# Kernel optimization log

Measured on AMD Instinct MI355X. Metric: run time of the kernel, lower is better.

Reference implementation:

```python
import jax, jax.numpy as jnp
import numpy as np

N, E, F_IN, EDIM, HEADS, DIM = 100000, 1600000, 128, 16, 4, 16
HC = HEADS * DIM


def add_self_loops_mean(src, dst, ea, n):
    # PyG add_self_loops with fill_value='mean': self-loop edge_attr is the mean
    # of incoming-edge attrs per target node (0 for isolated nodes).
    cnt = jax.ops.segment_sum(jnp.ones((dst.shape[0],), ea.dtype), dst, num_segments=n)
    sm = jax.ops.segment_sum(ea, dst, num_segments=n)
    loop = jnp.where(cnt[:, None] > 0, sm / jnp.maximum(cnt, 1.0)[:, None], 0.0)
    idx = jnp.arange(n, dtype=src.dtype)
    return (jnp.concatenate([src, idx]), jnp.concatenate([dst, idx]),
            jnp.concatenate([ea, loop], axis=0))


def gatv2(x, src, dst, ea, Wl, bl, Wr, br, We, att, bias):
    n = x.shape[0]
    h, c = att.shape
    xl = (x @ Wl + bl).reshape(n, h, c)   # source transform (lin_l)
    xr = (x @ Wr + br).reshape(n, h, c)   # target transform (lin_r)
    ee = (ea @ We).reshape(-1, h, c)      # edge transform (lin_edge, no bias)
    s = jax.nn.leaky_relu(xl[src] + xr[dst] + ee, negative_slope=0.2)  # [E,h,c]
    alpha = jnp.einsum('ehc,hc->eh', s, att)                           # [E,h]
    amax = jax.ops.segment_max(alpha, dst, num_segments=n)
    amax = jnp.where(jnp.isfinite(amax), amax, 0.0)
    ex = jnp.exp(alpha - amax[dst])
    denom = jax.ops.segment_sum(ex, dst, num_segments=n)
    a = ex / (denom[dst] + 1e-16)                                      # segment softmax
    out = jax.ops.segment_sum(xl[src] * a[:, :, None], dst, num_segments=n)
    return out.reshape(n, h * c) + bias


def setup_inputs() -> dict:
    key = jax.random.key(0)
    ks = jax.random.split(key, 24)
    s = 0.1
    d = {
        'x': jax.random.normal(ks[0], (N, F_IN), jnp.float32),
        'edge_index': jax.random.randint(ks[1], (2, E), 0, N, jnp.int32),
        'edge_attr': jax.random.normal(ks[2], (E, EDIM), jnp.float32),
        'Wl1': jax.random.normal(ks[3], (F_IN, HC)) * s, 'bl1': jnp.zeros((HC,)),
        'Wr1': jax.random.normal(ks[4], (F_IN, HC)) * s, 'br1': jnp.zeros((HC,)),
        'We1': jax.random.normal(ks[5], (EDIM, HC)) * s,
        'att1': jax.random.normal(ks[6], (HEADS, DIM)) * s,
        'bias1': jnp.zeros((HC,)),
        'Wl2': jax.random.normal(ks[7], (HC, HC)) * s, 'bl2': jnp.zeros((HC,)),
        'Wr2': jax.random.normal(ks[8], (HC, HC)) * s, 'br2': jnp.zeros((HC,)),
        'We2': jax.random.normal(ks[9], (EDIM, HC)) * s,
        'att2': jax.random.normal(ks[10], (HEADS, DIM)) * s,
        'bias2': jnp.zeros((HC,)),
        'W_lin1': jax.random.normal(ks[11], (HC, DIM)) * s, 'b_lin1': jnp.zeros((DIM,)),
        'W_lin2': jax.random.normal(ks[12], (DIM, 1)) * s, 'b_lin2': jnp.zeros((1,)),
    }
    return d


def reference(x, edge_index, edge_attr, Wl1, bl1, Wr1, br1, We1, att1, bias1,
              Wl2, bl2, Wr2, br2, We2, att2, bias2,
              W_lin1, b_lin1, W_lin2, b_lin2):
    src, dst, ea = add_self_loops_mean(edge_index[0], edge_index[1], edge_attr, x.shape[0])
    h = jax.nn.relu(gatv2(x, src, dst, ea, Wl1, bl1, Wr1, br1, We1, att1, bias1))
    h = jax.nn.relu(gatv2(h, src, dst, ea, Wl2, bl2, Wr2, br2, We2, att2, bias2))
    h = jax.nn.relu(h @ W_lin1 + b_lin1)
    # dropout p=0.1 is identity in eval mode
    out = jax.nn.sigmoid((h @ W_lin2 + b_lin2)[:, 0])
    return out
```

## Files before the change

### kernel.cpp

```cpp
#include <hip/hip_runtime.h>
#include <stdint.h>

typedef unsigned short u16;
typedef unsigned int u32;
typedef unsigned long long u64;

typedef __attribute__((ext_vector_type(8))) short bfrag;
typedef __attribute__((ext_vector_type(4))) float f32x4;
typedef __attribute__((ext_vector_type(2))) float f32x2;

__device__ __forceinline__ float bf2f(u16 u) { return __uint_as_float(((u32)u) << 16); }
__device__ __forceinline__ u16 f2bf(float f) {
    u32 i = __float_as_uint(f);
    u32 r = i + 0x7fffu + ((i >> 16) & 1u);
    return (u16)(r >> 16);
}
__device__ __forceinline__ float lo16(u32 u) { return __uint_as_float(u << 16); }
__device__ __forceinline__ float hi16(u32 u) { return __uint_as_float(u & 0xffff0000u); }
__device__ __forceinline__ u32 pack2(float a, float b) {
    return (u32)f2bf(a) | ((u32)f2bf(b) << 16);
}
#define RFL(x) __builtin_amdgcn_readfirstlane(x)

#define DPP_ROR_ADD(p, ctrl) \
    p += __int_as_float(__builtin_amdgcn_update_dpp(0, __float_as_int(p), ctrl, 0xF, 0xF, false))
__device__ __forceinline__ float red16(float p) {
    DPP_ROR_ADD(p, 0x128);
    DPP_ROR_ADD(p, 0x124);
    DPP_ROR_ADD(p, 0x122);
    DPP_ROR_ADD(p, 0x121);
    return p;
}

__global__ void deg_hist(const int* __restrict__ dst, int E, int* __restrict__ deg) {
    int e = blockIdx.x * blockDim.x + threadIdx.x;
    if (e < E) atomicAdd(&deg[dst[e]], 1);
}

#define SCAN_T 256
#define SCAN_E 8
#define SCAN_CHUNK 2048

__global__ void scan_partial(const int* __restrict__ deg, int n, int* __restrict__ partials) {
    __shared__ int sh[SCAN_T];
    int b = blockIdx.x, t = threadIdx.x;
    int base = b * SCAN_CHUNK + t * SCAN_E;
    int s = 0;
#pragma unroll
    for (int i = 0; i < SCAN_E; i++) { int idx = base + i; if (idx < n) s += deg[idx]; }
    sh[t] = s; __syncthreads();
    for (int off = SCAN_T / 2; off > 0; off >>= 1) {
        if (t < off) sh[t] += sh[t + off];
        __syncthreads();
    }
    if (t == 0) partials[b] = sh[0];
}

__global__ void scan_mid(int* __restrict__ partials, int nb) {
    if (threadIdx.x == 0 && blockIdx.x == 0) {
        int acc = 0;
        for (int i = 0; i < nb; i++) { int v = partials[i]; partials[i] = acc; acc += v; }
    }
}

__global__ void scan_final(const int* __restrict__ deg, int n, const int* __restrict__ partials,
                           int* __restrict__ offs, int E) {
    __shared__ int sh[SCAN_T];
    int b = blockIdx.x, t = threadIdx.x;
    int base = b * SCAN_CHUNK + t * SCAN_E;
    int loc[SCAN_E];
    int s = 0;
#pragma unroll
    for (int i = 0; i < SCAN_E; i++) {
        int idx = base + i;
        int v = (idx < n) ? deg[idx] : 0;
        loc[i] = s; s += v;
    }
    sh[t] = s; __syncthreads();
    for (int off = 1; off < SCAN_T; off <<= 1) {
        int v = 0;
        if (t >= off) v = sh[t - off];
        __syncthreads();
        if (t >= off) sh[t] += v;
        __syncthreads();
    }
    int tbase = partials[b] + sh[t] - s;
#pragma unroll
    for (int i = 0; i < SCAN_E; i++) { int idx = base + i; if (idx < n) offs[idx] = tbase + loc[i]; }
    if (b == gridDim.x - 1 && t == SCAN_T - 1) offs[n] = E;
}

__global__ void csr_fill_split(const int* __restrict__ srcv, const int* __restrict__ dstv,
                               const float4* __restrict__ ea, int E,
                               int* __restrict__ cursor,
                               int* __restrict__ csrc, float4* __restrict__ cattr) {
    int e = blockIdx.x * blockDim.x + threadIdx.x;
    if (e >= E) return;
    const float4* s = ea + (u64)e * 4;
    float4 v0 = s[0], v1 = s[1], v2 = s[2], v3 = s[3];
    int sr = srcv[e];
    int d = dstv[e];
    int p = atomicAdd(&cursor[d], 1);
    csrc[p] = sr;
    float4* dp = cattr + (u64)p * 4;
    dp[0] = v0; dp[1] = v1; dp[2] = v2; dp[3] = v3;
}

template <int K>
__global__ void pack_w(const float* __restrict__ Wl, const float* __restrict__ Wr,
                       u32* __restrict__ Wb) {
    constexpr int NKS = K / 32;
    int t = blockIdx.x * blockDim.x + threadIdx.x;
    if (t >= 8 * NKS * 64) return;
    int lane = t & 63;
    int ks = (t >> 6) % NKS;
    int ct = (t >> 6) / NKS;
    int n = lane & 15, quad = lane >> 4;
    int c = ct * 16 + n;
    const float* W = (c < 64) ? Wl : Wr;
    int cc = c & 63;
    u32* d = Wb + (u64)t * 4;
#pragma unroll
    for (int p = 0; p < 4; p++) {
        int k0 = ks * 32 + quad * 8 + 2 * p;
        d[p] = pack2(W[(u64)k0 * 64 + cc], W[(u64)(k0 + 1) * 64 + cc]);
    }
}

template <int K, bool XF32>
__global__ __launch_bounds__(256) void gemm_mfma(const void* __restrict__ Xv,
                                                 const u32* __restrict__ Wb,
                                                 const float* __restrict__ bl,
                                                 const float* __restrict__ br,
                                                 int N, u16* __restrict__ xl, u16* __restrict__ xr) {
    constexpr int NKS = K / 32;
    int lane = threadIdx.x & 63;
    int gw = (blockIdx.x * 256 + threadIdx.x) >> 6;
    int row0 = gw * 16;
    if (row0 >= N) return;
    int m = lane & 15, quad = lane >> 4;

    f32x4 acc[8];
#pragma unroll
    for (int ct = 0; ct < 8; ct++) acc[ct] = (f32x4){0.f, 0.f, 0.f, 0.f};

#pragma unroll
    for (int ks = 0; ks < NKS; ks++) {
        bfrag a;
        if (XF32) {
            const float* xp = (const float*)Xv + (u64)(row0 + m) * K + ks * 32 + quad * 8;
            float4 v0 = *(const float4*)xp;
            float4 v1 = *(const float4*)(xp + 4);
            union { bfrag v; u32 d[4]; } au;
            au.d[0] = pack2(v0.x, v0.y); au.d[1] = pack2(v0.z, v0.w);
            au.d[2] = pack2(v1.x, v1.y); au.d[3] = pack2(v1.z, v1.w);
            a = au.v;
        } else {
            a = *(const bfrag*)((const u16*)Xv + (u64)(row0 + m) * K + ks * 32 + quad * 8);
        }
#pragma unroll
        for (int ct = 0; ct < 8; ct++) {
            bfrag b = *(const bfrag*)(Wb + (u64)((ct * NKS + ks) * 64 + lane) * 4);
            acc[ct] = __builtin_amdgcn_mfma_f32_16x16x32_bf16(a, b, acc[ct], 0, 0, 0);
        }
    }

#pragma unroll
    for (int ct = 0; ct < 8; ct++) {
        float bv = (ct < 4) ? bl[ct * 16 + m] : br[(ct - 4) * 16 + m];
        u16* dbuf = (ct < 4) ? xl : xr;
        int cc = (ct & 3) * 16 + m;
#pragma unroll
        for (int r = 0; r < 4; r++) {
            int row = row0 + quad * 4 + r;
            dbuf[(u64)row * 64 + cc] = f2bf(acc[ct][r] + bv);
        }
    }
}

__global__ __launch_bounds__(256) void gat_layer(const u16* __restrict__ xl, const u16* __restrict__ xr,
                                                 const int* __restrict__ offs,
                                                 const int* __restrict__ csrc,
                                                 const float* __restrict__ cattr,
                                                 const float* __restrict__ We,
                                                 const float* __restrict__ att,
                                                 const float* __restrict__ bias,
                                                 int N, u16* __restrict__ out) {
    int l = threadIdx.x & 63;
    int wid = RFL((int)((blockIdx.x * 256 + threadIdx.x) >> 6));
    int nw = gridDim.x * 4;
    f32x2 wec2[8];
#pragma unroll
    for (int k = 0; k < 8; k++) {
        wec2[k].x = We[(2 * k) * 64 + l];
        wec2[k].y = We[(2 * k + 1) * 64 + l];
    }
    float att_ls = att[l] * 1.44269504088896340736f;
    float bias_l = bias[l];

    for (int n = wid; n < N; n += nw) {
        float xr_l = bf2f(xr[(u32)(n * 64 + l)]);
        float xl_self = bf2f(xl[(u32)(n * 64 + l)]);
        int a = RFL(offs[n]);
        int b = RFL(offs[n + 1]);

        float lsum0 = 0.f, lsum1 = 0.f, o0 = 0.f, o1 = 0.f, es0 = 0.f, es1 = 0.f;

        auto edge_c = [&](const float* eap, float xlv, float& lsum, float& o, float& eesum) {
            f32x2 e0 = {0.f, 0.f}, e1 = {0.f, 0.f};
#pragma unroll
            for (int k = 0; k < 4; k++) {
                f32x2 a0 = *(const f32x2*)(eap + 4 * k);
                f32x2 a1 = *(const f32x2*)(eap + 4 * k + 2);
                e0 = __builtin_elementwise_fma(a0, wec2[2 * k], e0);
                e1 = __builtin_elementwise_fma(a1, wec2[2 * k + 1], e1);
            }
            f32x2 es = e0 + e1;
            float eef = es.x + es.y;
            eesum += eef;
            float z = (eef + xr_l) + xlv;
            z = fmaxf(z, 0.2f * z);
            float vv = red16(z * att_ls);
            float w;
            asm("v_exp_f32 %0, %1" : "=v"(w) : "v"(vv));
            lsum += w;
            o = fmaf(w, xlv, o);
        };

        for (int base = a; base < b; base += 64) {
            int rem = b - base;
            int cnt = rem < 64 ? rem : 64;
            int idx = base + l;
            int sv = csrc[idx < b ? idx : (b - 1)];
            int j = 0;
            for (; j + 4 <= cnt; j += 4) {
                int s0 = __builtin_amdgcn_readlane(sv, j);
                int s1 = __builtin_amdgcn_readlane(sv, j + 1);
                int s2 = __builtin_amdgcn_readlane(sv, j + 2);
                int s3 = __builtin_amdgcn_readlane(sv, j + 3);
                float xlv0 = bf2f(xl[(u32)(s0 * 64 + l)]);
                float xlv1 = bf2f(xl[(u32)(s1 * 64 + l)]);
                float xlv2 = bf2f(xl[(u32)(s2 * 64 + l)]);
                float xlv3 = bf2f(xl[(u32)(s3 * 64 + l)]);
                const float* ep = cattr + (u64)(base + j) * 16;
                edge_c(ep,      xlv0, lsum0, o0, es0);
                edge_c(ep + 16, xlv1, lsum1, o1, es1);
                edge_c(ep + 32, xlv2, lsum0, o0, es0);
                edge_c(ep + 48, xlv3, lsum1, o1, es1);
            }
            for (; j < cnt; j++) {
                int s0 = __builtin_amdgcn_readlane(sv, j);
                float xlv0 = bf2f(xl[(u32)(s0 * 64 + l)]);
                edge_c(cattr + (u64)(base + j) * 16, xlv0, lsum0, o0, es0);
            }
        }

        float lsum = lsum0 + lsum1;
        float o = o0 + o1;
        float eesum = es0 + es1;

        {
            int deg = b - a;
            float inv = (deg > 0) ? 1.f / (float)deg : 0.f;
            float z = (eesum * inv + xr_l) + xl_self;
            z = fmaxf(z, 0.2f * z);
            float vv = red16(z * att_ls);
            float w;
            asm("v_exp_f32 %0, %1" : "=v"(w) : "v"(vv));
            lsum += w;
            o = fmaf(w, xl_self, o);
        }

        float res = o / (lsum + 1e-16f) + bias_l;
        res = fmaxf(res, 0.f);
        out[(u32)(n * 64 + l)] = f2bf(res);
    }
}

__global__ __launch_bounds__(256) void mlp_head(const u16* __restrict__ h,
                                                const float* __restrict__ W1, const float* __restrict__ b1,
                                                const float* __restrict__ W2, const float* __restrict__ b2,
                                                int N, float* __restrict__ out) {
    __shared__ float w1[64 * 16];
    __shared__ float sb1[16];
    __shared__ float w2[16];
    for (int i = threadIdx.x; i < 64 * 16; i += 256) w1[i] = W1[i];
    if (threadIdx.x < 16) { sb1[threadIdx.x] = b1[threadIdx.x]; w2[threadIdx.x] = W2[threadIdx.x]; }
    __syncthreads();
    float b2v = b2[0];
    int n = blockIdx.x * blockDim.x + threadIdx.x;
    if (n < N) {
        float hv[64];
        const u32* hp = (const u32*)(h + (u64)n * 64);
#pragma unroll
        for (int i = 0; i < 32; i++) { u32 u = hp[i]; hv[2 * i] = lo16(u); hv[2 * i + 1] = hi16(u); }
        float z = b2v;
        for (int j = 0; j < 16; j++) {
            float acc = sb1[j];
#pragma unroll
            for (int k = 0; k < 64; k++) acc = fmaf(hv[k], w1[k * 16 + j], acc);
            acc = fmaxf(acc, 0.f);
            z = fmaf(acc, w2[j], z);
        }
        out[n] = 1.f / (1.f + __expf(-z));
    }
}

extern "C" void kernel_launch(void* const* d_in, const int* in_sizes, int n_in,
                              void* d_out, int out_size, void* d_ws, size_t ws_size,
                              hipStream_t stream) {
    const float* x    = (const float*)d_in[0];
    const int*   ei   = (const int*)d_in[1];
    const float* ea   = (const float*)d_in[2];
    const float* Wl1  = (const float*)d_in[3];
    const float* bl1  = (const float*)d_in[4];
    const float* Wr1  = (const float*)d_in[5];
    const float* br1  = (const float*)d_in[6];
    const float* We1  = (const float*)d_in[7];
    const float* att1 = (const float*)d_in[8];
    const float* bias1= (const float*)d_in[9];
    const float* Wl2  = (const float*)d_in[10];
    const float* bl2  = (const float*)d_in[11];
    const float* Wr2  = (const float*)d_in[12];
    const float* br2  = (const float*)d_in[13];
    const float* We2  = (const float*)d_in[14];
    const float* att2 = (const float*)d_in[15];
    const float* bias2= (const float*)d_in[16];
    const float* W1   = (const float*)d_in[17];
    const float* b1   = (const float*)d_in[18];
    const float* W2   = (const float*)d_in[19];
    const float* b2   = (const float*)d_in[20];
    float* out = (float*)d_out;

    const int N = in_sizes[0] / 128;
    const int E = in_sizes[1] / 2;
    const int* srcv = ei;
    const int* dstv = ei + E;

    uint8_t* p = (uint8_t*)d_ws;
    auto carve = [&](size_t bytes) -> void* {
        void* r = (void*)p;
        p += (bytes + 255) & ~(size_t)255;
        return r;
    };
    int*  deg     = (int*)carve((size_t)N * 4);
    int*  cursor  = (int*)carve((size_t)N * 4);
    int*  offs    = (int*)carve((size_t)(N + 1) * 4);
    int*  partials= (int*)carve(4096);
    int*  csrc    = (int*)carve((size_t)E * 4);
    float* cattr  = (float*)carve((size_t)E * 64);
    u16*  xl      = (u16*)carve((size_t)N * 64 * 2);
    u16*  xr      = (u16*)carve((size_t)N * 64 * 2);
    u16*  hb      = (u16*)carve((size_t)N * 64 * 2);
    u32*  wb1     = (u32*)carve(8 * 4 * 64 * 16);
    u32*  wb2     = (u32*)carve(8 * 2 * 64 * 16);
    (void)ws_size; (void)n_in; (void)out_size;

    hipMemsetAsync(deg, 0, (size_t)N * 4, stream);

    const int B = 256;
    pack_w<128><<<8, 256, 0, stream>>>(Wl1, Wr1, wb1);
    pack_w<64><<<4, 256, 0, stream>>>(Wl2, Wr2, wb2);

    deg_hist<<<(E + B - 1) / B, B, 0, stream>>>(dstv, E, deg);
    int nb = (N + SCAN_CHUNK - 1) / SCAN_CHUNK;
    scan_partial<<<nb, SCAN_T, 0, stream>>>(deg, N, partials);
    scan_mid<<<1, 64, 0, stream>>>(partials, nb);
    scan_final<<<nb, SCAN_T, 0, stream>>>(deg, N, partials, offs, E);
    hipMemcpyAsync(cursor, offs, (size_t)N * 4, hipMemcpyDeviceToDevice, stream);
    csr_fill_split<<<(E + B - 1) / B, B, 0, stream>>>(srcv, dstv, (const float4*)ea, E,
                                                      cursor, csrc, (float4*)cattr);

    int gemm_blocks = (N / 16 + 3) / 4;
    gemm_mfma<128, true><<<gemm_blocks, 256, 0, stream>>>(x, wb1, bl1, br1, N, xl, xr);
    gat_layer<<<8192, 256, 0, stream>>>(xl, xr, offs, csrc, cattr,
                                        We1, att1, bias1, N, hb);
    gemm_mfma<64, false><<<gemm_blocks, 256, 0, stream>>>(hb, wb2, bl2, br2, N, xl, xr);
    gat_layer<<<8192, 256, 0, stream>>>(xl, xr, offs, csrc, cattr,
                                        We2, att2, bias2, N, hb);
    mlp_head<<<(N + B - 1) / B, B, 0, stream>>>(hb, W1, b1, W2, b2, N, out);
}
```

Before: 640.3 us.

## Use MFMA for edge projection in GAT layer, bf16 edge attrs, rank-based CSR fill

The GAT layer's per-edge edge-attribute projection moves onto MFMA bf16 instructions, with edges processed in groups of 16 and each lane handling one edge-row by channel-tile slice. Edge attributes are stored in the CSR as bf16, which halves their footprint and read traffic. The degree histogram now records each edge's rank, so the CSR fill computes positions directly instead of issuing a second atomic pass through a copied cursor array. In exchange, edge attributes lose precision, extra shuffles and cross-quad reductions are needed, and lanes are wasted when a node has few edges.

Result: no change. 631.8 us (-1.3%).

```diff
diff --git a/kernel.cpp b/kernel.cpp
--- a/kernel.cpp
+++ b/kernel.cpp
@@ -7,7 +7,6 @@
 
 typedef __attribute__((ext_vector_type(8))) short bfrag;
 typedef __attribute__((ext_vector_type(4))) float f32x4;
-typedef __attribute__((ext_vector_type(2))) float f32x2;
 
 __device__ __forceinline__ float bf2f(u16 u) { return __uint_as_float(((u32)u) << 16); }
 __device__ __forceinline__ u16 f2bf(float f) {
@@ -15,11 +14,11 @@
     u32 r = i + 0x7fffu + ((i >> 16) & 1u);
     return (u16)(r >> 16);
 }
+__device__ __forceinline__ u32 pack2(float a, float b) {
+    return (u32)f2bf(a) | ((u32)f2bf(b) << 16);
+}
 __device__ __forceinline__ float lo16(u32 u) { return __uint_as_float(u << 16); }
 __device__ __forceinline__ float hi16(u32 u) { return __uint_as_float(u & 0xffff0000u); }
-__device__ __forceinline__ u32 pack2(float a, float b) {
-    return (u32)f2bf(a) | ((u32)f2bf(b) << 16);
-}
 #define RFL(x) __builtin_amdgcn_readfirstlane(x)
 
 #define DPP_ROR_ADD(p, ctrl) \
@@ -32,9 +31,10 @@
     return p;
 }
 
-__global__ void deg_hist(const int* __restrict__ dst, int E, int* __restrict__ deg) {
+__global__ void rank_hist(const int* __restrict__ dst, int E,
+                          int* __restrict__ deg, int* __restrict__ rank) {
     int e = blockIdx.x * blockDim.x + threadIdx.x;
-    if (e < E) atomicAdd(&deg[dst[e]], 1);
+    if (e < E) rank[e] = atomicAdd(&deg[dst[e]], 1);
 }
 
 #define SCAN_T 256
@@ -91,19 +91,23 @@
 }
 
 __global__ void csr_fill_split(const int* __restrict__ srcv, const int* __restrict__ dstv,
+                               const int* __restrict__ rank,
+                               const int* __restrict__ offs,
                                const float4* __restrict__ ea, int E,
-                               int* __restrict__ cursor,
-                               int* __restrict__ csrc, float4* __restrict__ cattr) {
+                               int* __restrict__ csrc, uint4* __restrict__ cattr) {
     int e = blockIdx.x * blockDim.x + threadIdx.x;
     if (e >= E) return;
     const float4* s = ea + (u64)e * 4;
     float4 v0 = s[0], v1 = s[1], v2 = s[2], v3 = s[3];
-    int sr = srcv[e];
+    uint4 q0 = make_uint4(pack2(v0.x, v0.y), pack2(v0.z, v0.w),
+                          pack2(v1.x, v1.y), pack2(v1.z, v1.w));
+    uint4 q1 = make_uint4(pack2(v2.x, v2.y), pack2(v2.z, v2.w),
+                          pack2(v3.x, v3.y), pack2(v3.z, v3.w));
     int d = dstv[e];
-    int p = atomicAdd(&cursor[d], 1);
-    csrc[p] = sr;
-    float4* dp = cattr + (u64)p * 4;
-    dp[0] = v0; dp[1] = v1; dp[2] = v2; dp[3] = v3;
+    int p = offs[d] + rank[e];
+    csrc[p] = srcv[e];
+    cattr[(u64)p * 2] = q0;
+    cattr[(u64)p * 2 + 1] = q1;
 }
 
 template <int K>
@@ -127,6 +131,20 @@
     }
 }
 
+__global__ void pack_we(const float* __restrict__ We, u32* __restrict__ web) {
+    int t = blockIdx.x * blockDim.x + threadIdx.x;
+    if (t >= 256) return;
+    int lane = t & 63, ct = t >> 6;
+    int n = lane & 15, quad = lane >> 4;
+    int c = ct * 16 + n;
+    u32* d = web + (u64)t * 4;
+#pragma unroll
+    for (int p = 0; p < 4; p++) {
+        int k0 = quad * 8 + 2 * p;
+        d[p] = (k0 + 1 < 16) ? pack2(We[(u64)k0 * 64 + c], We[(u64)(k0 + 1) * 64 + c]) : 0u;
+    }
+}
+
 template <int K, bool XF32>
 __global__ __launch_bounds__(256) void gemm_mfma(const void* __restrict__ Xv,
                                                  const u32* __restrict__ Wb,
@@ -181,95 +199,135 @@
 __global__ __launch_bounds__(256) void gat_layer(const u16* __restrict__ xl, const u16* __restrict__ xr,
                                                  const int* __restrict__ offs,
                                                  const int* __restrict__ csrc,
-                                                 const float* __restrict__ cattr,
-                                                 const float* __restrict__ We,
+                                                 const u32* __restrict__ cattr,
+                                                 const u32* __restrict__ web,
                                                  const float* __restrict__ att,
                                                  const float* __restrict__ bias,
                                                  int N, u16* __restrict__ out) {
+    const float LOG2E = 1.44269504088896340736f;
     int l = threadIdx.x & 63;
+    int m = l & 15, quad = l >> 4;
     int wid = RFL((int)((blockIdx.x * 256 + threadIdx.x) >> 6));
     int nw = gridDim.x * 4;
-    f32x2 wec2[8];
-#pragma unroll
-    for (int k = 0; k < 8; k++) {
-        wec2[k].x = We[(2 * k) * 64 + l];
-        wec2[k].y = We[(2 * k + 1) * 64 + l];
-    }
-    float att_ls = att[l] * 1.44269504088896340736f;
+
+    bfrag wb[4];
+#pragma unroll
+    for (int ct = 0; ct < 4; ct++) wb[ct] = *(const bfrag*)(web + (u64)(ct * 64 + l) * 4);
+
+    float att_l = att[l] * LOG2E;
+    float att_f[4];
+#pragma unroll
+    for (int ct = 0; ct < 4; ct++) att_f[ct] = att[ct * 16 + m] * LOG2E;
     float bias_l = bias[l];
 
     for (int n = wid; n < N; n += nw) {
+        int a = RFL(offs[n]);
+        int b = RFL(offs[n + 1]);
         float xr_l = bf2f(xr[(u32)(n * 64 + l)]);
         float xl_self = bf2f(xl[(u32)(n * 64 + l)]);
-        int a = RFL(offs[n]);
-        int b = RFL(offs[n + 1]);
-
-        float lsum0 = 0.f, lsum1 = 0.f, o0 = 0.f, o1 = 0.f, es0 = 0.f, es1 = 0.f;
-
-        auto edge_c = [&](const float* eap, float xlv, float& lsum, float& o, float& eesum) {
-            f32x2 e0 = {0.f, 0.f}, e1 = {0.f, 0.f};
-#pragma unroll
-            for (int k = 0; k < 4; k++) {
-                f32x2 a0 = *(const f32x2*)(eap + 4 * k);
-                f32x2 a1 = *(const f32x2*)(eap + 4 * k + 2);
-                e0 = __builtin_elementwise_fma(a0, wec2[2 * k], e0);
-                e1 = __builtin_elementwise_fma(a1, wec2[2 * k + 1], e1);
+        float xr_f[4];
+#pragma unroll
+        for (int ct = 0; ct < 4; ct++) xr_f[ct] = bf2f(xr[(u32)(n * 64 + ct * 16 + m)]);
+
+        float o_f[4] = {0.f, 0.f, 0.f, 0.f};
+        float ls_f[4] = {0.f, 0.f, 0.f, 0.f};
+        float ee_f[4] = {0.f, 0.f, 0.f, 0.f};
+
+        for (int base = a; base < b; base += 64) {
+            int cnt64 = b - base; if (cnt64 > 64) cnt64 = 64;
+            int idx = base + l;
+            int sv = csrc[idx < b ? idx : b - 1];
+
+            for (int j = 0; j < cnt64; j += 16) {
+                int cnt = cnt64 - j; if (cnt > 16) cnt = 16;
+                union { bfrag v; u32 d[4]; } au;
+                au.d[0] = 0; au.d[1] = 0; au.d[2] = 0; au.d[3] = 0;
+                if (quad < 2 && m < cnt)
+                    au.v = *(const bfrag*)(cattr + (u64)(base + j + m) * 8 + quad * 4);
+                int jq = j + quad * 4;
+                int sr0 = __shfl(sv, jq);
+                int sr1 = __shfl(sv, jq + 1);
+                int sr2 = __shfl(sv, jq + 2);
+                int sr3 = __shfl(sv, jq + 3);
+                float xv[4][4];
+#pragma unroll
+                for (int ct = 0; ct < 4; ct++) {
+                    xv[0][ct] = bf2f(xl[(u32)(sr0 * 64 + ct * 16 + m)]);
+                    xv[1][ct] = bf2f(xl[(u32)(sr1 * 64 + ct * 16 + m)]);
+                    xv[2][ct] = bf2f(xl[(u32)(sr2 * 64 + ct * 16 + m)]);
+                    xv[3][ct] = bf2f(xl[(u32)(sr3 * 64 + ct * 16 + m)]);
+                }
+                f32x4 ee[4];
+#pragma unroll
+                for (int ct = 0; ct < 4; ct++) {
+                    f32x4 c = (f32x4){xr_f[ct], xr_f[ct], xr_f[ct], xr_f[ct]};
+                    ee[ct] = __builtin_amdgcn_mfma_f32_16x16x32_bf16(au.v, wb[ct], c, 0, 0, 0);
+                }
+#pragma unroll
+                for (int ct = 0; ct < 4; ct++)
+                    ee_f[ct] += (ee[ct][0] + ee[ct][1]) + (ee[ct][2] + ee[ct][3]) - 4.f * xr_f[ct];
+                float zz[4][4];
+#pragma unroll
+                for (int ct = 0; ct < 4; ct++) {
+#pragma unroll
+                    for (int r = 0; r < 4; r++) {
+                        float z = ee[ct][r] + xv[r][ct];
+                        z = fmaxf(z, 0.2f * z);
+                        zz[ct][r] = z * att_f[ct];
+                    }
+                }
+#define R16(ctrl) { \
+    DPP_ROR_ADD(zz[0][0], ctrl); DPP_ROR_ADD(zz[0][1], ctrl); DPP_ROR_ADD(zz[0][2], ctrl); DPP_ROR_ADD(zz[0][3], ctrl); \
+    DPP_ROR_ADD(zz[1][0], ctrl); DPP_ROR_ADD(zz[1][1], ctrl); DPP_ROR_ADD(zz[1][2], ctrl); DPP_ROR_ADD(zz[1][3], ctrl); \
+    DPP_ROR_ADD(zz[2][0], ctrl); DPP_ROR_ADD(zz[2][1], ctrl); DPP_ROR_ADD(zz[2][2], ctrl); DPP_ROR_ADD(zz[2][3], ctrl); \
+    DPP_ROR_ADD(zz[3][0], ctrl); DPP_ROR_ADD(zz[3][1], ctrl); DPP_ROR_ADD(zz[3][2], ctrl); DPP_ROR_ADD(zz[3][3], ctrl); }
+                R16(0x128) R16(0x124) R16(0x122) R16(0x121)
+#undef R16
+                float w[4][4];
+#pragma unroll
+                for (int ct = 0; ct < 4; ct++) {
+#pragma unroll
+                    for (int r = 0; r < 4; r++)
+                        asm("v_exp_f32 %0, %1" : "=v"(w[ct][r]) : "v"(zz[ct][r]));
+                }
+                if (cnt < 16) {
+#pragma unroll
+                    for (int r = 0; r < 4; r++) {
+                        bool ok = (quad * 4 + r) < cnt;
+#pragma unroll
+                        for (int ct = 0; ct < 4; ct++) w[ct][r] = ok ? w[ct][r] : 0.f;
+                    }
+                }
+#pragma unroll
+                for (int ct = 0; ct < 4; ct++) {
+#pragma unroll
+                    for (int r = 0; r < 4; r++) {
+                        ls_f[ct] += w[ct][r];
+                        o_f[ct] = fmaf(w[ct][r], xv[r][ct], o_f[ct]);
+                    }
+                }
             }
-            f32x2 es = e0 + e1;
-            float eef = es.x + es.y;
-            eesum += eef;
-            float z = (eef + xr_l) + xlv;
-            z = fmaxf(z, 0.2f * z);
-            float vv = red16(z * att_ls);
-            float w;
-            asm("v_exp_f32 %0, %1" : "=v"(w) : "v"(vv));
-            lsum += w;
-            o = fmaf(w, xlv, o);
-        };
-
-        for (int base = a; base < b; base += 64) {
-            int rem = b - base;
-            int cnt = rem < 64 ? rem : 64;
-            int idx = base + l;
-            int sv = csrc[idx < b ? idx : (b - 1)];
-            int j = 0;
-            for (; j + 4 <= cnt; j += 4) {
-                int s0 = __builtin_amdgcn_readlane(sv, j);
-                int s1 = __builtin_amdgcn_readlane(sv, j + 1);
-                int s2 = __builtin_amdgcn_readlane(sv, j + 2);
-                int s3 = __builtin_amdgcn_readlane(sv, j + 3);
-                float xlv0 = bf2f(xl[(u32)(s0 * 64 + l)]);
-                float xlv1 = bf2f(xl[(u32)(s1 * 64 + l)]);
-                float xlv2 = bf2f(xl[(u32)(s2 * 64 + l)]);
-                float xlv3 = bf2f(xl[(u32)(s3 * 64 + l)]);
-                const float* ep = cattr + (u64)(base + j) * 16;
-                edge_c(ep,      xlv0, lsum0, o0, es0);
-                edge_c(ep + 16, xlv1, lsum1, o1, es1);
-                edge_c(ep + 32, xlv2, lsum0, o0, es0);
-                edge_c(ep + 48, xlv3, lsum1, o1, es1);
-            }
-            for (; j < cnt; j++) {
-                int s0 = __builtin_amdgcn_readlane(sv, j);
-                float xlv0 = bf2f(xl[(u32)(s0 * 64 + l)]);
-                edge_c(cattr + (u64)(base + j) * 16, xlv0, lsum0, o0, es0);
-            }
-        }
-
-        float lsum = lsum0 + lsum1;
-        float o = o0 + o1;
-        float eesum = es0 + es1;
-
-        {
-            int deg = b - a;
-            float inv = (deg > 0) ? 1.f / (float)deg : 0.f;
-            float z = (eesum * inv + xr_l) + xl_self;
-            z = fmaxf(z, 0.2f * z);
-            float vv = red16(z * att_ls);
-            float w;
-            asm("v_exp_f32 %0, %1" : "=v"(w) : "v"(vv));
-            lsum += w;
-            o = fmaf(w, xl_self, o);
-        }
+        }
+
+#pragma unroll
+        for (int ct = 0; ct < 4; ct++) {
+            o_f[ct] += __shfl_xor(o_f[ct], 16);  o_f[ct] += __shfl_xor(o_f[ct], 32);
+            ls_f[ct] += __shfl_xor(ls_f[ct], 16); ls_f[ct] += __shfl_xor(ls_f[ct], 32);
+            ee_f[ct] += __shfl_xor(ee_f[ct], 16); ee_f[ct] += __shfl_xor(ee_f[ct], 32);
+        }
+        float o    = (quad & 2) ? ((quad & 1) ? o_f[3] : o_f[2]) : ((quad & 1) ? o_f[1] : o_f[0]);
+        float lsum = (quad & 2) ? ((quad & 1) ? ls_f[3] : ls_f[2]) : ((quad & 1) ? ls_f[1] : ls_f[0]);
+        float eesum= (quad & 2) ? ((quad & 1) ? ee_f[3] : ee_f[2]) : ((quad & 1) ? ee_f[1] : ee_f[0]);
+
+        int deg = b - a;
+        float inv = (deg > 0) ? 1.f / (float)deg : 0.f;
+        float z = (eesum * inv + xr_l) + xl_self;
+        z = fmaxf(z, 0.2f * z);
+        float vv = red16(z * att_l);
+        float ws;
+        asm("v_exp_f32 %0, %1" : "=v"(ws) : "v"(vv));
+        lsum += ws;
+        o = fmaf(ws, xl_self, o);
 
         float res = o / (lsum + 1e-16f) + bias_l;
         res = fmaxf(res, 0.f);
@@ -344,16 +402,18 @@
         return r;
     };
     int*  deg     = (int*)carve((size_t)N * 4);
-    int*  cursor  = (int*)carve((size_t)N * 4);
+    int*  rank    = (int*)carve((size_t)E * 4);
     int*  offs    = (int*)carve((size_t)(N + 1) * 4);
     int*  partials= (int*)carve(4096);
     int*  csrc    = (int*)carve((size_t)E * 4);
-    float* cattr  = (float*)carve((size_t)E * 64);
+    u32*  cattr   = (u32*)carve((size_t)E * 32);
     u16*  xl      = (u16*)carve((size_t)N * 64 * 2);
     u16*  xr      = (u16*)carve((size_t)N * 64 * 2);
     u16*  hb      = (u16*)carve((size_t)N * 64 * 2);
     u32*  wb1     = (u32*)carve(8 * 4 * 64 * 16);
     u32*  wb2     = (u32*)carve(8 * 2 * 64 * 16);
+    u32*  web1    = (u32*)carve(4 * 64 * 4 * 4);
+    u32*  web2    = (u32*)carve(4 * 64 * 4 * 4);
     (void)ws_size; (void)n_in; (void)out_size;
 
     hipMemsetAsync(deg, 0, (size_t)N * 4, stream);
@@ -361,22 +421,23 @@
     const int B = 256;
     pack_w<128><<<8, 256, 0, stream>>>(Wl1, Wr1, wb1);
     pack_w<64><<<4, 256, 0, stream>>>(Wl2, Wr2, wb2);
-
-    deg_hist<<<(E + B - 1) / B, B, 0, stream>>>(dstv, E, deg);
+    pack_we<<<1, 256, 0, stream>>>(We1, web1);
+    pack_we<<<1, 256, 0, stream>>>(We2, web2);
+
+    rank_hist<<<(E + B - 1) / B, B, 0, stream>>>(dstv, E, deg, rank);
     int nb = (N + SCAN_CHUNK - 1) / SCAN_CHUNK;
     scan_partial<<<nb, SCAN_T, 0, stream>>>(deg, N, partials);
     scan_mid<<<1, 64, 0, stream>>>(partials, nb);
     scan_final<<<nb, SCAN_T, 0, stream>>>(deg, N, partials, offs, E);
-    hipMemcpyAsync(cursor, offs, (size_t)N * 4, hipMemcpyDeviceToDevice, stream);
-    csr_fill_split<<<(E + B - 1) / B, B, 0, stream>>>(srcv, dstv, (const float4*)ea, E,
-                                                      cursor, csrc, (float4*)cattr);
+    csr_fill_split<<<(E + B - 1) / B, B, 0, stream>>>(srcv, dstv, rank, offs,
+                                                      (const float4*)ea, E, csrc, (uint4*)cattr);
 
     int gemm_blocks = (N / 16 + 3) / 4;
     gemm_mfma<128, true><<<gemm_blocks, 256, 0, stream>>>(x, wb1, bl1, br1, N, xl, xr);
-    gat_layer<<<8192, 256, 0, stream>>>(xl, xr, offs, csrc, cattr,
-                                        We1, att1, bias1, N, hb);
+    gat_layer<<<8192, 256, 0, stream>>>(xl, xr, offs, csrc, cattr, web1,
+                                        att1, bias1, N, hb);
     gemm_mfma<64, false><<<gemm_blocks, 256, 0, stream>>>(hb, wb2, bl2, br2, N, xl, xr);
-    gat_layer<<<8192, 256, 0, stream>>>(xl, xr, offs, csrc, cattr,
-                                        We2, att2, bias2, N, hb);
+    gat_layer<<<8192, 256, 0, stream>>>(xl, xr, offs, csrc, cattr, web2,
+                                        att2, bias2, N, hb);
     mlp_head<<<(N + B - 1) / B, B, 0, stream>>>(hb, W1, b1, W2, b2, N, out);
 }
```
